# Optimization experiments

Hardware: AMD Instinct MI355X
Metric: run time of the kernel (lower is better)

## Reference

```python
import jax, jax.numpy as jnp
import numpy as np

K3, R, N_IN, N_OUT, C_IN, C_OUT = 27, 1_000_000, 2_000_000, 2_000_000, 32, 32


def setup_inputs() -> dict:
    key = jax.random.key(0)
    k0, k1, k2, k3, k4 = jax.random.split(key, 5)
    x_data = jax.random.normal(k0, (N_IN, C_IN), dtype=jnp.float32)
    # kaiming_normal_ fan_out for weights of shape [K3, C_in, C_out]
    std = np.float32(np.sqrt(2.0 / (K3 * C_OUT)))
    weights = jax.random.normal(k1, (K3, C_IN, C_OUT), dtype=jnp.float32) * std
    bias = jax.random.normal(k2, (C_OUT,), dtype=jnp.float32)
    in_inds = jax.random.randint(k3, (K3, R), 0, N_IN, dtype=jnp.int32)
    out_inds = jax.random.randint(k4, (K3, R), 0, N_OUT, dtype=jnp.int32)
    return {
        "x_data": x_data,
        "weights": weights,
        "bias": bias,
        "in_inds": in_inds,
        "out_inds": out_inds,
        "n_out": N_OUT,
    }


def reference(x_data, weights, bias, in_inds, out_inds, n_out):
    # Rulebook gather -> matmul -> scatter-add per kernel offset.
    # scan over the K3 kernel-offset axis keeps peak memory to one offset's
    # gathered block ([R, C_in]) instead of materializing all K3 at once.
    c_out = weights.shape[-1]
    out0 = jnp.zeros((n_out, c_out), dtype=x_data.dtype)

    def step(acc, offset):
        w, ii, oi = offset                      # [C_in,C_out], [R], [R]
        gathered = x_data[ii]                   # [R, C_in] gather
        acc = acc.at[oi].add(gathered @ w)      # scatter-add [R, C_out]
        return acc, None

    out, _ = jax.lax.scan(step, out0, (weights, in_inds, out_inds))
    return out + bias[None, :]
```

## Files before the change

### kernel.cpp

```cpp
#include <hip/hip_runtime.h>


#define K3    27
#define RULES 1000000
#define CIN   32
#define COUT  32
#define NOUT  2000000

__global__ __launch_bounds__(256) void bias_init_kernel(
    float* __restrict__ out, const float* __restrict__ bias) {
  float4 b[8];
#pragma unroll
  for (int j = 0; j < 8; ++j)
    b[j] = reinterpret_cast<const float4*>(bias)[j];
  const size_t total4 = (size_t)NOUT * COUT / 4;
  const size_t stride = (size_t)gridDim.x * blockDim.x;
  for (size_t i = (size_t)blockIdx.x * blockDim.x + threadIdx.x; i < total4;
       i += stride) {
    reinterpret_cast<float4*>(out)[i] = b[i & 7];
  }
}

__global__ __launch_bounds__(256) void scatter_gemm_kernel(
    const float* __restrict__ x, const float* __restrict__ weights,
    const int* __restrict__ in_inds, const int* __restrict__ out_inds,
    float* __restrict__ out) {
  const int k    = blockIdx.y;
  const int e    = blockIdx.x * 256 + threadIdx.x;
  const int wave = threadIdx.x >> 6;
  const int lane = threadIdx.x & 63;

  __shared__ float sacc[4][64][33];
  __shared__ int   soi[4][64];

  const bool valid = (e < RULES);
  int ii = 0, oi = -1;
  if (valid) {
    ii = in_inds[(size_t)k * RULES + e];
    oi = out_inds[(size_t)k * RULES + e];
  }

  float xr[CIN];
  if (valid) {
    const float4* __restrict__ xrow =
        reinterpret_cast<const float4*>(x + (size_t)ii * CIN);
#pragma unroll
    for (int j = 0; j < 8; ++j) {
      float4 v = xrow[j];
      xr[4 * j + 0] = v.x;
      xr[4 * j + 1] = v.y;
      xr[4 * j + 2] = v.z;
      xr[4 * j + 3] = v.w;
    }
  } else {
#pragma unroll
    for (int j = 0; j < CIN; ++j) xr[j] = 0.f;
  }

  float acc[COUT];
#pragma unroll
  for (int c = 0; c < COUT; ++c) acc[c] = 0.f;

  const float* __restrict__ wk = weights + (size_t)k * CIN * COUT;
#pragma unroll
  for (int i = 0; i < CIN; ++i) {
    const float xi = xr[i];
#pragma unroll
    for (int c = 0; c < COUT; ++c) acc[c] += xi * wk[i * COUT + c];
  }

#pragma unroll
  for (int c = 0; c < COUT; ++c) sacc[wave][lane][c] = acc[c];
  if (lane < 64) soi[wave][lane] = oi;
  __syncthreads();

  const int half = lane >> 5;
  const int c    = lane & 31;
#pragma unroll
  for (int it = 0; it < 32; ++it) {
    const int eidx = it * 2 + half;
    const int o    = soi[wave][eidx];
    if (o >= 0) {
      atomicAdd(&out[(size_t)o * COUT + c], sacc[wave][eidx][c]);
    }
  }
}

extern "C" void kernel_launch(void* const* d_in, const int* in_sizes, int n_in,
                              void* d_out, int out_size, void* d_ws,
                              size_t ws_size, hipStream_t stream) {
  const float* x       = (const float*)d_in[0];
  const float* weights = (const float*)d_in[1];
  const float* bias    = (const float*)d_in[2];
  const int*   in_inds = (const int*)d_in[3];
  const int*   out_inds= (const int*)d_in[4];
  float*       out     = (float*)d_out;

  bias_init_kernel<<<2048, 256, 0, stream>>>(out, bias);

  dim3 grid((RULES + 255) / 256, K3);
  scatter_gemm_kernel<<<grid, 256, 0, stream>>>(x, weights, in_inds, out_inds,
                                                out);
}
```

Baseline: 2.790 ms.

## Bucket rules by output tile and accumulate in LDS instead of global atomics

Replaces the global-atomic scatter with a counting-sort pipeline. It histograms rules by (offset, 256-row output tile), scans the counts and places packed in/out indices into buckets. A gather kernel then processes one output tile per block, accumulating in shared memory with LDS atomics and writing each output row once with the bias added. This removes about 864M global float atomics and the separate bias-init pass, at the cost of extra passes over the indices, more workspace, and serialized per-wave loops over variable-length bins. If the workspace is too small it falls back to a simplified direct-atomic kernel.

After: 7.703 ms. +176.1%, slower.

```diff
diff --git a/kernel.cpp b/kernel.cpp
--- a/kernel.cpp
+++ b/kernel.cpp
@@ -6,99 +6,255 @@
 #define CIN   32
 #define COUT  32
 #define NOUT  2000000
+#define TR    256
+#define NT    ((NOUT + TR - 1) / TR)
+#define NBINS (K3 * NT)
+#define SCAN_CHUNK 2048
+#define NSCAN ((NBINS + SCAN_CHUNK - 1) / SCAN_CHUNK)
+
+__global__ __launch_bounds__(256) void hist_kernel(
+    const int* __restrict__ out_inds, int* __restrict__ cnt) {
+  const int k = blockIdx.y;
+  const int e = blockIdx.x * 256 + threadIdx.x;
+  if (e < RULES) {
+    const int oi = out_inds[(size_t)k * RULES + e];
+    atomicAdd(&cnt[k * NT + (oi >> 8)], 1);
+  }
+}
+
+__global__ __launch_bounds__(256) void scan1_kernel(
+    const int* __restrict__ cnt, int* __restrict__ offs,
+    int* __restrict__ partials) {
+  __shared__ int sd[256];
+  const int t = threadIdx.x;
+  const int base = blockIdx.x * SCAN_CHUNK + t * 8;
+  int v[8];
+  int s = 0;
+#pragma unroll
+  for (int i = 0; i < 8; ++i) {
+    const int idx = base + i;
+    v[i] = (idx < NBINS) ? cnt[idx] : 0;
+    s += v[i];
+  }
+  sd[t] = s;
+  __syncthreads();
+  const int own = s;
+  for (int d = 1; d < 256; d <<= 1) {
+    const int xx = (t >= d) ? sd[t - d] : 0;
+    __syncthreads();
+    sd[t] += xx;
+    __syncthreads();
+  }
+  const int excl = sd[t] - own;
+  if (t == 255) partials[blockIdx.x] = sd[255];
+  int run = excl;
+#pragma unroll
+  for (int i = 0; i < 8; ++i) {
+    const int idx = base + i;
+    if (idx < NBINS) offs[idx] = run;
+    run += v[i];
+  }
+}
+
+__global__ __launch_bounds__(256) void scan2_kernel(int* __restrict__ partials) {
+  __shared__ int sd[256];
+  const int t = threadIdx.x;
+  const int own = (t < NSCAN) ? partials[t] : 0;
+  sd[t] = own;
+  __syncthreads();
+  for (int d = 1; d < 256; d <<= 1) {
+    const int xx = (t >= d) ? sd[t - d] : 0;
+    __syncthreads();
+    sd[t] += xx;
+    __syncthreads();
+  }
+  if (t < NSCAN) partials[t] = sd[t] - own;
+}
+
+__global__ __launch_bounds__(256) void scan3_kernel(
+    int* __restrict__ offs, const int* __restrict__ partials,
+    int* __restrict__ cursor) {
+  const int base = blockIdx.x * SCAN_CHUNK + threadIdx.x * 8;
+  const int add = partials[blockIdx.x];
+#pragma unroll
+  for (int i = 0; i < 8; ++i) {
+    const int idx = base + i;
+    if (idx < NBINS) {
+      const int v = offs[idx] + add;
+      offs[idx] = v;
+      cursor[idx] = v;
+    }
+  }
+}
+
+__global__ __launch_bounds__(256) void place_kernel(
+    const int* __restrict__ in_inds, const int* __restrict__ out_inds,
+    int* __restrict__ cursor, unsigned* __restrict__ entries) {
+  const int k = blockIdx.y;
+  const int e = blockIdx.x * 256 + threadIdx.x;
+  if (e >= RULES) return;
+  const size_t idx = (size_t)k * RULES + e;
+  const int oi = out_inds[idx];
+  const int ii = in_inds[idx];
+  const int bin = k * NT + (oi >> 8);
+  const int pos = atomicAdd(&cursor[bin], 1);
+  entries[pos] = ((unsigned)ii << 8) | (unsigned)(oi & 255);
+}
+
+__global__ __launch_bounds__(512) void gather_kernel(
+    const float* __restrict__ x, const float* __restrict__ weights,
+    const float* __restrict__ bias, const int* __restrict__ offs,
+    const int* __restrict__ cnt, const unsigned* __restrict__ entries,
+    float* __restrict__ out) {
+  __shared__ float sacc[TR * COUT];
+  const int bt = blockIdx.x;
+  const int tid = threadIdx.x;
+
+#pragma unroll
+  for (int r = 0; r < 4; ++r)
+    reinterpret_cast<float4*>(sacc)[r * 512 + tid] = make_float4(0.f, 0.f, 0.f, 0.f);
+  __syncthreads();
+
+  const int wave = tid >> 6;
+  const int lane = tid & 63;
+  const int q = lane >> 4;
+  const int c2 = lane & 15;
+  const float4* __restrict__ xb = reinterpret_cast<const float4*>(x);
+
+  for (int kk = wave; kk < K3; kk += 8) {
+    const int bin = kk * NT + bt;
+    int s = __builtin_amdgcn_readfirstlane(offs[bin]);
+    int n = __builtin_amdgcn_readfirstlane(cnt[bin]);
+    if (n == 0) continue;
+
+    float2 w2[8];
+    const float2* __restrict__ wp =
+        reinterpret_cast<const float2*>(weights + (size_t)kk * CIN * COUT);
+#pragma unroll
+    for (int i = 0; i < 8; ++i) w2[i] = wp[(q * 8 + i) * 16 + c2];
+
+    const int jend = s + n;
+    unsigned u0 = (unsigned)__builtin_amdgcn_readfirstlane((int)entries[s]);
+    float4 a0 = xb[(size_t)(u0 >> 8) * 8 + 2 * q];
+    float4 b0 = xb[(size_t)(u0 >> 8) * 8 + 2 * q + 1];
+    for (int j = s; j < jend; ++j) {
+      const int jn = (j + 1 < jend) ? (j + 1) : j;
+      const unsigned u1 =
+          (unsigned)__builtin_amdgcn_readfirstlane((int)entries[jn]);
+      const float4 a1 = xb[(size_t)(u1 >> 8) * 8 + 2 * q];
+      const float4 b1 = xb[(size_t)(u1 >> 8) * 8 + 2 * q + 1];
+
+      const int ol = (int)(u0 & 255u);
+      float ax = 0.f, ay = 0.f;
+      ax += a0.x * w2[0].x; ay += a0.x * w2[0].y;
+      ax += a0.y * w2[1].x; ay += a0.y * w2[1].y;
+      ax += a0.z * w2[2].x; ay += a0.z * w2[2].y;
+      ax += a0.w * w2[3].x; ay += a0.w * w2[3].y;
+      ax += b0.x * w2[4].x; ay += b0.x * w2[4].y;
+      ax += b0.y * w2[5].x; ay += b0.y * w2[5].y;
+      ax += b0.z * w2[6].x; ay += b0.z * w2[6].y;
+      ax += b0.w * w2[7].x; ay += b0.w * w2[7].y;
+      ax += __shfl_xor(ax, 16); ay += __shfl_xor(ay, 16);
+      ax += __shfl_xor(ax, 32); ay += __shfl_xor(ay, 32);
+      if (lane < 16) {
+        atomicAdd(&sacc[ol * COUT + 2 * c2], ax);
+        atomicAdd(&sacc[ol * COUT + 2 * c2 + 1], ay);
+      }
+      u0 = u1; a0 = a1; b0 = b1;
+    }
+  }
+  __syncthreads();
+
+  const float4* __restrict__ b4 = reinterpret_cast<const float4*>(bias);
+#pragma unroll
+  for (int r = 0; r < 4; ++r) {
+    const int idx = r * 512 + tid;
+    const int row = idx >> 3;
+    const int f4c = idx & 7;
+    const int grow = bt * TR + row;
+    if (grow < NOUT) {
+      float4 v = reinterpret_cast<float4*>(sacc)[idx];
+      const float4 bb = b4[f4c];
+      v.x += bb.x; v.y += bb.y; v.z += bb.z; v.w += bb.w;
+      reinterpret_cast<float4*>(out)[(size_t)grow * 8 + f4c] = v;
+    }
+  }
+}
 
 __global__ __launch_bounds__(256) void bias_init_kernel(
     float* __restrict__ out, const float* __restrict__ bias) {
   float4 b[8];
 #pragma unroll
-  for (int j = 0; j < 8; ++j)
-    b[j] = reinterpret_cast<const float4*>(bias)[j];
+  for (int j = 0; j < 8; ++j) b[j] = reinterpret_cast<const float4*>(bias)[j];
   const size_t total4 = (size_t)NOUT * COUT / 4;
   const size_t stride = (size_t)gridDim.x * blockDim.x;
   for (size_t i = (size_t)blockIdx.x * blockDim.x + threadIdx.x; i < total4;
-       i += stride) {
+       i += stride)
     reinterpret_cast<float4*>(out)[i] = b[i & 7];
-  }
 }
 
 __global__ __launch_bounds__(256) void scatter_gemm_kernel(
     const float* __restrict__ x, const float* __restrict__ weights,
     const int* __restrict__ in_inds, const int* __restrict__ out_inds,
     float* __restrict__ out) {
-  const int k    = blockIdx.y;
-  const int e    = blockIdx.x * 256 + threadIdx.x;
-  const int wave = threadIdx.x >> 6;
-  const int lane = threadIdx.x & 63;
-
-  __shared__ float sacc[4][64][33];
-  __shared__ int   soi[4][64];
-
-  const bool valid = (e < RULES);
-  int ii = 0, oi = -1;
-  if (valid) {
-    ii = in_inds[(size_t)k * RULES + e];
-    oi = out_inds[(size_t)k * RULES + e];
-  }
-
+  const int k = blockIdx.y;
+  const int e = blockIdx.x * 256 + threadIdx.x;
+  if (e >= RULES) return;
+  const int ii = in_inds[(size_t)k * RULES + e];
+  const int oi = out_inds[(size_t)k * RULES + e];
   float xr[CIN];
-  if (valid) {
-    const float4* __restrict__ xrow =
-        reinterpret_cast<const float4*>(x + (size_t)ii * CIN);
-#pragma unroll
-    for (int j = 0; j < 8; ++j) {
-      float4 v = xrow[j];
-      xr[4 * j + 0] = v.x;
-      xr[4 * j + 1] = v.y;
-      xr[4 * j + 2] = v.z;
-      xr[4 * j + 3] = v.w;
-    }
-  } else {
-#pragma unroll
-    for (int j = 0; j < CIN; ++j) xr[j] = 0.f;
-  }
-
+  const float4* xrow = reinterpret_cast<const float4*>(x + (size_t)ii * CIN);
+#pragma unroll
+  for (int j = 0; j < 8; ++j) {
+    float4 v = xrow[j];
+    xr[4 * j] = v.x; xr[4 * j + 1] = v.y; xr[4 * j + 2] = v.z; xr[4 * j + 3] = v.w;
+  }
+  const float* wk = weights + (size_t)k * CIN * COUT;
   float acc[COUT];
 #pragma unroll
   for (int c = 0; c < COUT; ++c) acc[c] = 0.f;
-
-  const float* __restrict__ wk = weights + (size_t)k * CIN * COUT;
 #pragma unroll
   for (int i = 0; i < CIN; ++i) {
     const float xi = xr[i];
 #pragma unroll
     for (int c = 0; c < COUT; ++c) acc[c] += xi * wk[i * COUT + c];
   }
-
-#pragma unroll
-  for (int c = 0; c < COUT; ++c) sacc[wave][lane][c] = acc[c];
-  if (lane < 64) soi[wave][lane] = oi;
-  __syncthreads();
-
-  const int half = lane >> 5;
-  const int c    = lane & 31;
-#pragma unroll
-  for (int it = 0; it < 32; ++it) {
-    const int eidx = it * 2 + half;
-    const int o    = soi[wave][eidx];
-    if (o >= 0) {
-      atomicAdd(&out[(size_t)o * COUT + c], sacc[wave][eidx][c]);
-    }
-  }
+#pragma unroll
+  for (int c = 0; c < COUT; ++c) atomicAdd(&out[(size_t)oi * COUT + c], acc[c]);
 }
 
 extern "C" void kernel_launch(void* const* d_in, const int* in_sizes, int n_in,
                               void* d_out, int out_size, void* d_ws,
                               size_t ws_size, hipStream_t stream) {
-  const float* x       = (const float*)d_in[0];
-  const float* weights = (const float*)d_in[1];
-  const float* bias    = (const float*)d_in[2];
-  const int*   in_inds = (const int*)d_in[3];
-  const int*   out_inds= (const int*)d_in[4];
-  float*       out     = (float*)d_out;
-
-  bias_init_kernel<<<2048, 256, 0, stream>>>(out, bias);
-
-  dim3 grid((RULES + 255) / 256, K3);
-  scatter_gemm_kernel<<<grid, 256, 0, stream>>>(x, weights, in_inds, out_inds,
-                                                out);
-}
+  const float* x        = (const float*)d_in[0];
+  const float* weights  = (const float*)d_in[1];
+  const float* bias     = (const float*)d_in[2];
+  const int*   in_inds  = (const int*)d_in[3];
+  const int*   out_inds = (const int*)d_in[4];
+  float*       out      = (float*)d_out;
+
+  int* cnt      = (int*)d_ws;
+  int* offs     = cnt + NBINS;
+  int* cursor   = offs + NBINS;
+  int* partials = cursor + NBINS;
+  unsigned* entries = (unsigned*)(partials + 128);
+  const size_t REQ = ((size_t)3 * NBINS + 128 + (size_t)K3 * RULES) * 4;
+
+  if (ws_size < REQ) {
+    bias_init_kernel<<<2048, 256, 0, stream>>>(out, bias);
+    dim3 grid((RULES + 255) / 256, K3);
+    scatter_gemm_kernel<<<grid, 256, 0, stream>>>(x, weights, in_inds,
+                                                  out_inds, out);
+    return;
+  }
+
+  hipMemsetAsync(cnt, 0, (size_t)NBINS * sizeof(int), stream);
+  dim3 rgrid((RULES + 255) / 256, K3);
+  hist_kernel<<<rgrid, 256, 0, stream>>>(out_inds, cnt);
+  scan1_kernel<<<NSCAN, 256, 0, stream>>>(cnt, offs, partials);
+  scan2_kernel<<<1, 256, 0, stream>>>(partials);
+  scan3_kernel<<<NSCAN, 256, 0, stream>>>(offs, partials, cursor);
+  place_kernel<<<rgrid, 256, 0, stream>>>(in_inds, out_inds, cursor, entries);
+  gather_kernel<<<NT, 512, 0, stream>>>(x, weights, bias, offs, cnt, entries,
+                                        out);
+}
```
